# Kernel tuning notes

Hardware: AMD Instinct MI355X
Metric: run time of the kernel (lower is better)

Reference implementation:

```python
import jax, jax.numpy as jnp
import numpy as np
from jax.scipy.special import logsumexp

REG_E = 0.05
N_ITER = 20


def setup_inputs() -> dict:
    key = jax.random.key(0)
    kP, kQ = jax.random.split(key)
    n, m, d = 8192, 8192, 64
    XP = jax.random.normal(kP, (n, d), dtype=jnp.float32)
    XQ = jax.random.normal(kQ, (m, d), dtype=jnp.float32)
    return {"XP": XP, "XQ": XQ}


def sq_cdist(X, Y):
    # squared euclidean distances, (n, m)
    x2 = jnp.sum(X * X, axis=1, keepdims=True)          # (n,1)
    y2 = jnp.sum(Y * Y, axis=1, keepdims=True).T        # (1,m)
    d2 = x2 + y2 - 2.0 * (X @ Y.T)
    return jnp.maximum(d2, 0.0)


def log_sinkhorn(log_a, log_b, C, reg, n_iter):
    # stable log-domain Sinkhorn; returns transport plan exp(M + u[:,None] + v[None,:])
    M = -C / reg                                        # (n,m)
    u0 = jnp.zeros_like(log_a)
    v0 = jnp.zeros_like(log_b)

    def body(carry, _):
        u, v = carry
        u = log_a - logsumexp(M + v[None, :], axis=1)
        v = log_b - logsumexp(M + u[:, None], axis=0)
        return (u, v), None

    (u, v), _ = jax.lax.scan(body, (u0, v0), None, length=n_iter)
    return jnp.exp(M + u[:, None] + v[None, :])


def reference(XP, XQ):
    n, m = XP.shape[0], XQ.shape[0]
    log_uP = jnp.full((n,), -jnp.log(jnp.float32(n)), dtype=XP.dtype)
    log_uQ = jnp.full((m,), -jnp.log(jnp.float32(m)), dtype=XQ.dtype)

    C = sq_cdist(XP, XQ)                                # (n, m)
    Cn = C / jax.lax.stop_gradient(jnp.max(C))
    plan = jax.lax.stop_gradient(
        log_sinkhorn(log_uP, log_uQ, Cn, REG_E, N_ITER)
    )
    return jnp.sum(C * plan)
```

## Files before the change

kernel.cpp:

```cpp
#include <hip/hip_runtime.h>
#include <cmath>

#define NPTS 8192
#define DIM  64
#define LOG2E 1.4426950408889634f
#define LA2   -13.0f

typedef short s16x8  __attribute__((ext_vector_type(8)));
typedef float f32x16 __attribute__((ext_vector_type(16)));

typedef __attribute__((address_space(1))) const unsigned char g8_t;
typedef __attribute__((address_space(3))) unsigned char l8_t;

#if __has_builtin(__builtin_amdgcn_exp2f)
__device__ __forceinline__ float exp2_fast(float x) { return __builtin_amdgcn_exp2f(x); }
#else
__device__ __forceinline__ float exp2_fast(float x) { return exp2f(x); }
#endif
#if __has_builtin(__builtin_amdgcn_logf)
__device__ __forceinline__ float log2_fast(float x) { return __builtin_amdgcn_logf(x); }
#else
__device__ __forceinline__ float log2_fast(float x) { return log2f(x); }
#endif

__device__ __forceinline__ unsigned short f2bf(float x) {
  unsigned u = __float_as_uint(x);
  return (unsigned short)((u + 0x7FFFu + ((u >> 16) & 1u)) >> 16);
}
__device__ __forceinline__ float bf2f(unsigned short b) {
  return __uint_as_float(((unsigned)b) << 16);
}

__global__ __launch_bounds__(256) void prep_kernel(
    const float* __restrict__ XP, const float* __restrict__ XQ,
    unsigned short* __restrict__ Phi, unsigned short* __restrict__ Plo,
    unsigned short* __restrict__ Qhi, unsigned short* __restrict__ Qlo,
    float* __restrict__ x2, float* __restrict__ y2,
    float* __restrict__ scal, float* __restrict__ out) {
  int gid  = blockIdx.x * 256 + threadIdx.x;
  int lane = threadIdx.x & 63;
  int row  = gid >> 6;
  int isP  = row < NPTS;
  int r    = row & (NPTS - 1);
  const float* X = isP ? XP : XQ;
  float x = X[r * DIM + lane];
  unsigned short h = f2bf(x);
  (isP ? Phi : Qhi)[r * DIM + lane] = h;
  (isP ? Plo : Qlo)[r * DIM + lane] = f2bf(x - bf2f(h));
  float s = x * x;
  for (int off = 32; off; off >>= 1) s += __shfl_down(s, off, 64);
  if (lane == 0) (isP ? x2 : y2)[r] = s;
  if (gid == 0) { ((unsigned*)scal)[0] = 0u; out[0] = 0.0f; }
}

template <int MODE, bool FIRST, int MINW>
__global__ __launch_bounds__(256, MINW) void pass_kernel(
    const unsigned short* __restrict__ Ahi, const unsigned short* __restrict__ Alo,
    const unsigned short* __restrict__ Bhi,
    const float* __restrict__ x2row, const float* __restrict__ y2col,
    const float* __restrict__ colPart, const float* __restrict__ rowPart,
    const unsigned* __restrict__ cmaxBits,
    float* __restrict__ outPart, float* __restrict__ outScalar) {
  __shared__ short sB[2][128 * DIM];
  __shared__ float sCol[512];
  __shared__ float sY2[512];
  __shared__ float sX2[128];
  __shared__ float sU2[128];
  __shared__ float sRed[4];

  const int t  = threadIdx.x;
  const int w  = t >> 6;
  const int l  = t & 63;
  const int g  = l >> 5;
  const int ln = l & 31;
  const int i0 = blockIdx.x * 128;
  const int j0 = blockIdx.y * 512;

  float invC = 0.f, C2L = 0.f;
  if constexpr (MODE != 0) {
    float cmax = __uint_as_float(*cmaxBits);
    invC = 1.0f / (0.05f * cmax);
    C2L  = 2.0f * invC * LOG2E;
  }

  const int gOff   = (w * 32 + (l >> 3)) * 128 + (((l & 7) ^ (l >> 3)) * 16);
  const int ldsOff = w * 4096 + l * 16;
  auto stage = [&](int qq, int bi) {
    const unsigned char* src =
        (const unsigned char*)(Bhi + (size_t)(j0 + qq * 128) * DIM) + gOff;
    unsigned char* dst = (unsigned char*)(&sB[bi][0]) + ldsOff;
#pragma unroll
    for (int c = 0; c < 4; ++c)
      __builtin_amdgcn_global_load_lds((g8_t*)(src + c * 1024),
                                       (l8_t*)(dst + c * 1024), 16, 0, 0);
  };

  stage(0, 0);
  stage(1, 1);

  s16x8 a_hi[4], a_lo[4];
  {
    const unsigned short* pa = Ahi + (size_t)(i0 + w * 32 + ln) * DIM + g * 8;
#pragma unroll
    for (int ks = 0; ks < 4; ++ks) a_hi[ks] = *(const s16x8*)(pa + ks * 16);
    if constexpr (MODE == 2) {
      const unsigned short* pb = Alo + (size_t)(i0 + w * 32 + ln) * DIM + g * 8;
#pragma unroll
      for (int ks = 0; ks < 4; ++ks) a_lo[ks] = *(const s16x8*)(pb + ks * 16);
    }
  }

#pragma unroll
  for (int c0 = 0; c0 < 2; ++c0) {
    int c = c0 * 256 + t;
    int j = j0 + c;
    if constexpr (MODE == 0) {
      sY2[c] = y2col[j];
    } else if constexpr (MODE == 1) {
      if constexpr (FIRST) {
        sCol[c] = -invC * y2col[j] * LOG2E;
      } else {
        float s = 0.f;
#pragma unroll
        for (int gy = 0; gy < 16; ++gy) s += colPart[gy * NPTS + j];
        sCol[c] = LA2 - log2_fast(s);
      }
    } else {
      float s = 0.f;
#pragma unroll
      for (int gy = 0; gy < 16; ++gy) s += colPart[gy * NPTS + j];
      sCol[c] = LA2 - log2_fast(s);
      sY2[c] = y2col[j];
    }
  }
  if constexpr (MODE != 1) {
    if (t < 128) {
      sX2[t] = x2row[i0 + t];
      if constexpr (MODE == 2) {
        float s = 0.f;
#pragma unroll
        for (int gy = 0; gy < 16; ++gy) s += rowPart[gy * NPTS + i0 + t];
        sU2[t] = LA2 - log2_fast(s);
      }
    }
  }
  __syncthreads();

  float x2r[16], u2r[16];
  if constexpr (MODE != 1) {
#pragma unroll
    for (int r = 0; r < 16; ++r) {
      int ri = w * 32 + (r & 3) + 8 * (r >> 2) + 4 * g;
      x2r[r] = sX2[ri];
      if constexpr (MODE == 2) u2r[r] = sU2[ri];
    }
  }

  float racc[16];
#pragma unroll
  for (int r = 0; r < 16; ++r) racc[r] = 0.f;
  float accS = 0.f;

  auto do_quarter = [&](const short* __restrict__ buf, int qq) {
#pragma unroll 2
    for (int ct = 0; ct < 4; ++ct) {
      const int nn = ct * 32 + ln;
      const int n  = qq * 128 + ct * 32 + ln;
      s16x8 b[4];
#pragma unroll
      for (int ks = 0; ks < 4; ++ks)
        b[ks] = *(const s16x8*)(buf + nn * DIM + (((ks * 2 + g) ^ (ln & 7)) * 8));
      f32x16 acc;
#pragma unroll
      for (int r = 0; r < 16; ++r) acc[r] = 0.f;
#pragma unroll
      for (int ks = 0; ks < 4; ++ks)
        acc = __builtin_amdgcn_mfma_f32_32x32x16_bf16(a_hi[ks], b[ks], acc, 0, 0, 0);

      if constexpr (MODE == 1) {
        const float bb = sCol[n];
#pragma unroll
        for (int r = 0; r < 16; ++r)
          racc[r] += exp2_fast(fmaf(C2L, acc[r], bb));
      } else if constexpr (MODE == 0) {
        const float y2v = sY2[n];
#pragma unroll
        for (int r = 0; r < 16; ++r)
          accS = fmaxf(accS, fmaf(-2.0f, acc[r], x2r[r] + y2v));
      } else {
        f32x16 acc2;
#pragma unroll
        for (int r = 0; r < 16; ++r) acc2[r] = 0.f;
#pragma unroll
        for (int ks = 0; ks < 4; ++ks)
          acc2 = __builtin_amdgcn_mfma_f32_32x32x16_bf16(a_lo[ks], b[ks], acc2, 0, 0, 0);
        const float y2v = sY2[n];
        const float bb  = sCol[n];
#pragma unroll
        for (int r = 0; r < 16; ++r) {
          float dot = acc[r] + acc2[r];
          float d2  = fmaxf(fmaf(-2.0f, dot, x2r[r] + y2v), 0.0f);
          accS = fmaf(d2, exp2_fast(fmaf(C2L, dot, u2r[r] + bb)), accS);
        }
      }
    }
  };

  do_quarter(sB[0], 0);
  __syncthreads();
  stage(2, 0);
  do_quarter(sB[1], 1);
  __syncthreads();
  stage(3, 1);
  do_quarter(sB[0], 2);
  __syncthreads();
  do_quarter(sB[1], 3);

  if constexpr (MODE == 1) {
#pragma unroll
    for (int r = 0; r < 16; ++r) {
      float v = racc[r];
      v += __shfl_xor(v, 1, 64);
      v += __shfl_xor(v, 2, 64);
      v += __shfl_xor(v, 4, 64);
      v += __shfl_xor(v, 8, 64);
      v += __shfl_xor(v, 16, 64);
      if (ln == 0)
        outPart[blockIdx.y * NPTS + i0 + w * 32 +
                (r & 3) + 8 * (r >> 2) + 4 * g] = v;
    }
  } else {
    float v = accS;
#pragma unroll
    for (int off = 1; off < 64; off <<= 1) {
      float o = __shfl_xor(v, off, 64);
      v = (MODE == 0) ? fmaxf(v, o) : (v + o);
    }
    if (l == 0) sRed[w] = v;
    __syncthreads();
    if (t == 0) {
      float r0 = (MODE == 0) ? fmaxf(fmaxf(sRed[0], sRed[1]), fmaxf(sRed[2], sRed[3]))
                             : (sRed[0] + sRed[1] + sRed[2] + sRed[3]);
      if constexpr (MODE == 0)
        atomicMax((unsigned*)outScalar, __float_as_uint(r0));
      else
        atomicAdd(outScalar, r0);
    }
  }
}

extern "C" void kernel_launch(void* const* d_in, const int* in_sizes, int n_in,
                              void* d_out, int out_size, void* d_ws, size_t ws_size,
                              hipStream_t stream) {
  (void)in_sizes; (void)n_in; (void)out_size; (void)ws_size;
  const float* XP = (const float*)d_in[0];
  const float* XQ = (const float*)d_in[1];
  float* out = (float*)d_out;

  float* ws    = (float*)d_ws;
  float* x2    = ws;
  float* y2    = ws + 8192;
  float* partU = ws + 16384;
  float* partV = partU + 16 * NPTS;
  float* scal  = partV + 16 * NPTS;
  unsigned short* Phi = (unsigned short*)(scal + 16);
  unsigned short* Plo = Phi + (size_t)NPTS * DIM;
  unsigned short* Qhi = Plo + (size_t)NPTS * DIM;
  unsigned short* Qlo = Qhi + (size_t)NPTS * DIM;

  const unsigned* cmaxB = (const unsigned*)scal;
  dim3 grid(NPTS / 128, NPTS / 512);

  prep_kernel<<<NPTS * 2 * DIM / 256, 256, 0, stream>>>(
      XP, XQ, Phi, Plo, Qhi, Qlo, x2, y2, scal, out);

  pass_kernel<0, false, 4><<<grid, 256, 0, stream>>>(
      Phi, nullptr, Qhi, x2, y2, nullptr, nullptr, cmaxB, nullptr, scal);

  pass_kernel<1, true, 4><<<grid, 256, 0, stream>>>(
      Phi, nullptr, Qhi, nullptr, y2, nullptr, nullptr, cmaxB, partU, nullptr);
  pass_kernel<1, false, 4><<<grid, 256, 0, stream>>>(
      Qhi, nullptr, Phi, nullptr, nullptr, partU, nullptr, cmaxB, partV, nullptr);

  for (int it = 1; it < 20; ++it) {
    pass_kernel<1, false, 4><<<grid, 256, 0, stream>>>(
        Phi, nullptr, Qhi, nullptr, nullptr, partV, nullptr, cmaxB, partU, nullptr);
    pass_kernel<1, false, 4><<<grid, 256, 0, stream>>>(
        Qhi, nullptr, Phi, nullptr, nullptr, partU, nullptr, cmaxB, partV, nullptr);
  }

  pass_kernel<2, false, 2><<<grid, 256, 0, stream>>>(
      Phi, Plo, Qhi, x2, y2, partV, partU, cmaxB, nullptr, out);
}
```

Measured before the change: 820.2 us.

## Process two row strips per block to reuse staged column tiles

Each block of the distance-max and Sinkhorn passes now covers 256 rows instead of 128. It keeps two sets of A fragments and row accumulators in registers, so each B tile loaded into LDS and read into registers feeds twice the MFMA work. The grid for those passes is halved and the launch-bounds occupancy hint drops from 4 to 2, trading fewer waves and more registers for less LDS staging and LDS reads per output. The final weighted-sum pass keeps the single-strip layout.

```diff
diff --git a/kernel.cpp b/kernel.cpp
--- a/kernel.cpp
+++ b/kernel.cpp
@@ -53,7 +53,7 @@
   if (gid == 0) { ((unsigned*)scal)[0] = 0u; out[0] = 0.0f; }
 }
 
-template <int MODE, bool FIRST, int MINW>
+template <int MODE, bool FIRST, int MINW, int STRIPS>
 __global__ __launch_bounds__(256, MINW) void pass_kernel(
     const unsigned short* __restrict__ Ahi, const unsigned short* __restrict__ Alo,
     const unsigned short* __restrict__ Bhi,
@@ -64,7 +64,7 @@
   __shared__ short sB[2][128 * DIM];
   __shared__ float sCol[512];
   __shared__ float sY2[512];
-  __shared__ float sX2[128];
+  __shared__ float sX2[256];
   __shared__ float sU2[128];
   __shared__ float sRed[4];
 
@@ -73,7 +73,7 @@
   const int l  = t & 63;
   const int g  = l >> 5;
   const int ln = l & 31;
-  const int i0 = blockIdx.x * 128;
+  const int i0 = blockIdx.x * (128 * STRIPS);
   const int j0 = blockIdx.y * 512;
 
   float invC = 0.f, C2L = 0.f;
@@ -98,15 +98,18 @@
   stage(0, 0);
   stage(1, 1);
 
-  s16x8 a_hi[4], a_lo[4];
-  {
-    const unsigned short* pa = Ahi + (size_t)(i0 + w * 32 + ln) * DIM + g * 8;
-#pragma unroll
-    for (int ks = 0; ks < 4; ++ks) a_hi[ks] = *(const s16x8*)(pa + ks * 16);
+  s16x8 a_hi[STRIPS][4], a_lo[STRIPS][4];
+#pragma unroll
+  for (int s = 0; s < STRIPS; ++s) {
+    const unsigned short* pa =
+        Ahi + (size_t)(i0 + s * 128 + w * 32 + ln) * DIM + g * 8;
+#pragma unroll
+    for (int ks = 0; ks < 4; ++ks) a_hi[s][ks] = *(const s16x8*)(pa + ks * 16);
     if constexpr (MODE == 2) {
-      const unsigned short* pb = Alo + (size_t)(i0 + w * 32 + ln) * DIM + g * 8;
-#pragma unroll
-      for (int ks = 0; ks < 4; ++ks) a_lo[ks] = *(const s16x8*)(pb + ks * 16);
+      const unsigned short* pb =
+          Alo + (size_t)(i0 + s * 128 + w * 32 + ln) * DIM + g * 8;
+#pragma unroll
+      for (int ks = 0; ks < 4; ++ks) a_lo[s][ks] = *(const s16x8*)(pb + ks * 16);
     }
   }
 
@@ -134,7 +137,7 @@
     }
   }
   if constexpr (MODE != 1) {
-    if (t < 128) {
+    if (t < 128 * STRIPS) {
       sX2[t] = x2row[i0 + t];
       if constexpr (MODE == 2) {
         float s = 0.f;
@@ -146,19 +149,23 @@
   }
   __syncthreads();
 
-  float x2r[16], u2r[16];
+  float x2r[STRIPS][16], u2r[STRIPS][16];
   if constexpr (MODE != 1) {
 #pragma unroll
-    for (int r = 0; r < 16; ++r) {
-      int ri = w * 32 + (r & 3) + 8 * (r >> 2) + 4 * g;
-      x2r[r] = sX2[ri];
-      if constexpr (MODE == 2) u2r[r] = sU2[ri];
-    }
-  }
-
-  float racc[16];
-#pragma unroll
-  for (int r = 0; r < 16; ++r) racc[r] = 0.f;
+    for (int s = 0; s < STRIPS; ++s)
+#pragma unroll
+      for (int r = 0; r < 16; ++r) {
+        int ri = s * 128 + w * 32 + (r & 3) + 8 * (r >> 2) + 4 * g;
+        x2r[s][r] = sX2[ri];
+        if constexpr (MODE == 2) u2r[s][r] = sU2[ri];
+      }
+  }
+
+  float racc[STRIPS][16];
+#pragma unroll
+  for (int s = 0; s < STRIPS; ++s)
+#pragma unroll
+    for (int r = 0; r < 16; ++r) racc[s][r] = 0.f;
   float accS = 0.f;
 
   auto do_quarter = [&](const short* __restrict__ buf, int qq) {
@@ -170,37 +177,40 @@
 #pragma unroll
       for (int ks = 0; ks < 4; ++ks)
         b[ks] = *(const s16x8*)(buf + nn * DIM + (((ks * 2 + g) ^ (ln & 7)) * 8));
-      f32x16 acc;
-#pragma unroll
-      for (int r = 0; r < 16; ++r) acc[r] = 0.f;
-#pragma unroll
-      for (int ks = 0; ks < 4; ++ks)
-        acc = __builtin_amdgcn_mfma_f32_32x32x16_bf16(a_hi[ks], b[ks], acc, 0, 0, 0);
-
-      if constexpr (MODE == 1) {
-        const float bb = sCol[n];
-#pragma unroll
-        for (int r = 0; r < 16; ++r)
-          racc[r] += exp2_fast(fmaf(C2L, acc[r], bb));
-      } else if constexpr (MODE == 0) {
-        const float y2v = sY2[n];
-#pragma unroll
-        for (int r = 0; r < 16; ++r)
-          accS = fmaxf(accS, fmaf(-2.0f, acc[r], x2r[r] + y2v));
-      } else {
-        f32x16 acc2;
-#pragma unroll
-        for (int r = 0; r < 16; ++r) acc2[r] = 0.f;
+#pragma unroll
+      for (int s = 0; s < STRIPS; ++s) {
+        f32x16 acc;
+#pragma unroll
+        for (int r = 0; r < 16; ++r) acc[r] = 0.f;
 #pragma unroll
         for (int ks = 0; ks < 4; ++ks)
-          acc2 = __builtin_amdgcn_mfma_f32_32x32x16_bf16(a_lo[ks], b[ks], acc2, 0, 0, 0);
-        const float y2v = sY2[n];
-        const float bb  = sCol[n];
-#pragma unroll
-        for (int r = 0; r < 16; ++r) {
-          float dot = acc[r] + acc2[r];
-          float d2  = fmaxf(fmaf(-2.0f, dot, x2r[r] + y2v), 0.0f);
-          accS = fmaf(d2, exp2_fast(fmaf(C2L, dot, u2r[r] + bb)), accS);
+          acc = __builtin_amdgcn_mfma_f32_32x32x16_bf16(a_hi[s][ks], b[ks], acc, 0, 0, 0);
+
+        if constexpr (MODE == 1) {
+          const float bb = sCol[n];
+#pragma unroll
+          for (int r = 0; r < 16; ++r)
+            racc[s][r] += exp2_fast(fmaf(C2L, acc[r], bb));
+        } else if constexpr (MODE == 0) {
+          const float y2v = sY2[n];
+#pragma unroll
+          for (int r = 0; r < 16; ++r)
+            accS = fmaxf(accS, fmaf(-2.0f, acc[r], x2r[s][r] + y2v));
+        } else {
+          f32x16 acc2;
+#pragma unroll
+          for (int r = 0; r < 16; ++r) acc2[r] = 0.f;
+#pragma unroll
+          for (int ks = 0; ks < 4; ++ks)
+            acc2 = __builtin_amdgcn_mfma_f32_32x32x16_bf16(a_lo[s][ks], b[ks], acc2, 0, 0, 0);
+          const float y2v = sY2[n];
+          const float bb  = sCol[n];
+#pragma unroll
+          for (int r = 0; r < 16; ++r) {
+            float dot = acc[r] + acc2[r];
+            float d2  = fmaxf(fmaf(-2.0f, dot, x2r[s][r] + y2v), 0.0f);
+            accS = fmaf(d2, exp2_fast(fmaf(C2L, dot, u2r[s][r] + bb)), accS);
+          }
         }
       }
     }
@@ -218,17 +228,19 @@
 
   if constexpr (MODE == 1) {
 #pragma unroll
-    for (int r = 0; r < 16; ++r) {
-      float v = racc[r];
-      v += __shfl_xor(v, 1, 64);
-      v += __shfl_xor(v, 2, 64);
-      v += __shfl_xor(v, 4, 64);
-      v += __shfl_xor(v, 8, 64);
-      v += __shfl_xor(v, 16, 64);
-      if (ln == 0)
-        outPart[blockIdx.y * NPTS + i0 + w * 32 +
-                (r & 3) + 8 * (r >> 2) + 4 * g] = v;
-    }
+    for (int s = 0; s < STRIPS; ++s)
+#pragma unroll
+      for (int r = 0; r < 16; ++r) {
+        float v = racc[s][r];
+        v += __shfl_xor(v, 1, 64);
+        v += __shfl_xor(v, 2, 64);
+        v += __shfl_xor(v, 4, 64);
+        v += __shfl_xor(v, 8, 64);
+        v += __shfl_xor(v, 16, 64);
+        if (ln == 0)
+          outPart[blockIdx.y * NPTS + i0 + s * 128 + w * 32 +
+                  (r & 3) + 8 * (r >> 2) + 4 * g] = v;
+      }
   } else {
     float v = accS;
 #pragma unroll
@@ -269,26 +281,27 @@
   unsigned short* Qlo = Qhi + (size_t)NPTS * DIM;
 
   const unsigned* cmaxB = (const unsigned*)scal;
-  dim3 grid(NPTS / 128, NPTS / 512);
+  dim3 grid2(NPTS / 256, NPTS / 512);
+  dim3 grid1(NPTS / 128, NPTS / 512);
 
   prep_kernel<<<NPTS * 2 * DIM / 256, 256, 0, stream>>>(
       XP, XQ, Phi, Plo, Qhi, Qlo, x2, y2, scal, out);
 
-  pass_kernel<0, false, 4><<<grid, 256, 0, stream>>>(
+  pass_kernel<0, false, 2, 2><<<grid2, 256, 0, stream>>>(
       Phi, nullptr, Qhi, x2, y2, nullptr, nullptr, cmaxB, nullptr, scal);
 
-  pass_kernel<1, true, 4><<<grid, 256, 0, stream>>>(
+  pass_kernel<1, true, 2, 2><<<grid2, 256, 0, stream>>>(
       Phi, nullptr, Qhi, nullptr, y2, nullptr, nullptr, cmaxB, partU, nullptr);
-  pass_kernel<1, false, 4><<<grid, 256, 0, stream>>>(
+  pass_kernel<1, false, 2, 2><<<grid2, 256, 0, stream>>>(
       Qhi, nullptr, Phi, nullptr, nullptr, partU, nullptr, cmaxB, partV, nullptr);
 
   for (int it = 1; it < 20; ++it) {
-    pass_kernel<1, false, 4><<<grid, 256, 0, stream>>>(
+    pass_kernel<1, false, 2, 2><<<grid2, 256, 0, stream>>>(
         Phi, nullptr, Qhi, nullptr, nullptr, partV, nullptr, cmaxB, partU, nullptr);
-    pass_kernel<1, false, 4><<<grid, 256, 0, stream>>>(
+    pass_kernel<1, false, 2, 2><<<grid2, 256, 0, stream>>>(
         Qhi, nullptr, Phi, nullptr, nullptr, partU, nullptr, cmaxB, partV, nullptr);
   }
 
-  pass_kernel<2, false, 2><<<grid, 256, 0, stream>>>(
+  pass_kernel<2, false, 2, 1><<<grid1, 256, 0, stream>>>(
       Phi, Plo, Qhi, x2, y2, partV, partU, cmaxB, nullptr, out);
 }
```

Result: slower. 943.9 us (+15.1%).

## Split Sinkhorn sum pass into lean kernel with smaller column tiles

Applied to the files above, without the earlier changes.

Moves the Sinkhorn logsumexp pass (MODE 1) into a dedicated sum_kernel that uses half-width column tiles (256 per block), half the LDS, per-k B fragment loads and launch bounds targeting 8 waves per SIMD. The grid doubles in y, so the partial-sum buffers grow from 16 to 32 slices and every consumer now reduces 32 partials. The goal is higher occupancy and less register and LDS pressure, so exp2 work overlaps better with the MFMAs. In exchange there are more partial writes and reads, A-fragment loads are repeated across twice as many blocks, and there is less reuse per block.

```diff
diff --git a/kernel.cpp b/kernel.cpp
--- a/kernel.cpp
+++ b/kernel.cpp
@@ -53,6 +53,112 @@
   if (gid == 0) { ((unsigned*)scal)[0] = 0u; out[0] = 0.0f; }
 }
 
+template <bool FIRST>
+__global__ __launch_bounds__(256, 8) void sum_kernel(
+    const unsigned short* __restrict__ Ahi,
+    const unsigned short* __restrict__ Bhi,
+    const float* __restrict__ y2col,
+    const float* __restrict__ colPart,
+    const unsigned* __restrict__ cmaxBits,
+    float* __restrict__ outPart) {
+  __shared__ short sB[2][64 * DIM];
+  __shared__ float sCol[256];
+
+  const int t  = threadIdx.x;
+  const int w  = t >> 6;
+  const int l  = t & 63;
+  const int g  = l >> 5;
+  const int ln = l & 31;
+  const int i0 = blockIdx.x * 128;
+  const int j0 = blockIdx.y * 256;
+
+  const float cmax = __uint_as_float(*cmaxBits);
+  const float invC = 1.0f / (0.05f * cmax);
+  const float C2L  = 2.0f * invC * LOG2E;
+
+  const int gOff   = (w * 16 + (l >> 3)) * 128 + (((l & 7) ^ (l >> 3)) * 16);
+  const int ldsOff = w * 2048 + l * 16;
+  auto stage = [&](int qq, int bi) {
+    const unsigned char* src =
+        (const unsigned char*)(Bhi + (size_t)(j0 + qq * 64) * DIM) + gOff;
+    unsigned char* dst = (unsigned char*)(&sB[bi][0]) + ldsOff;
+#pragma unroll
+    for (int c = 0; c < 2; ++c)
+      __builtin_amdgcn_global_load_lds((g8_t*)(src + c * 1024),
+                                       (l8_t*)(dst + c * 1024), 16, 0, 0);
+  };
+
+  stage(0, 0);
+  stage(1, 1);
+
+  s16x8 a_hi[4];
+  {
+    const unsigned short* pa = Ahi + (size_t)(i0 + w * 32 + ln) * DIM + g * 8;
+#pragma unroll
+    for (int ks = 0; ks < 4; ++ks) a_hi[ks] = *(const s16x8*)(pa + ks * 16);
+  }
+
+  {
+    int j = j0 + t;
+    if constexpr (FIRST) {
+      sCol[t] = -invC * y2col[j] * LOG2E;
+    } else {
+      float s = 0.f;
+#pragma unroll
+      for (int gy = 0; gy < 32; ++gy) s += colPart[gy * NPTS + j];
+      sCol[t] = LA2 - log2_fast(s);
+    }
+  }
+  __syncthreads();
+
+  float racc[16];
+#pragma unroll
+  for (int r = 0; r < 16; ++r) racc[r] = 0.f;
+
+  auto do_quarter = [&](const short* __restrict__ buf, int qq) {
+#pragma unroll 1
+    for (int ct = 0; ct < 2; ++ct) {
+      const int nn = ct * 32 + ln;
+      const int n  = qq * 64 + ct * 32 + ln;
+      f32x16 acc;
+#pragma unroll
+      for (int r = 0; r < 16; ++r) acc[r] = 0.f;
+#pragma unroll
+      for (int ks = 0; ks < 4; ++ks) {
+        s16x8 b = *(const s16x8*)(buf + nn * DIM + (((ks * 2 + g) ^ (ln & 7)) * 8));
+        acc = __builtin_amdgcn_mfma_f32_32x32x16_bf16(a_hi[ks], b, acc, 0, 0, 0);
+      }
+      const float bb = sCol[n];
+#pragma unroll
+      for (int r = 0; r < 16; ++r)
+        racc[r] += exp2_fast(fmaf(C2L, acc[r], bb));
+    }
+  };
+
+  do_quarter(sB[0], 0);
+  __syncthreads();
+  stage(2, 0);
+  do_quarter(sB[1], 1);
+  __syncthreads();
+  stage(3, 1);
+  do_quarter(sB[0], 2);
+  __syncthreads();
+  do_quarter(sB[1], 3);
+
+#pragma unroll
+  for (int r = 0; r < 16; ++r) {
+    float v = racc[r];
+    v += __shfl_xor(v, 1, 64);
+    v += __shfl_xor(v, 2, 64);
+    v += __shfl_xor(v, 4, 64);
+    v += __shfl_xor(v, 8, 64);
+    v += __shfl_xor(v, 16, 64);
+    if (ln == 0)
+      outPart[blockIdx.y * NPTS + i0 + w * 32 +
+              (r & 3) + 8 * (r >> 2) + 4 * g] = v;
+  }
+}
+
 template <int MODE, bool FIRST, int MINW>
 __global__ __launch_bounds__(256, MINW) void pass_kernel(
     const unsigned short* __restrict__ Ahi, const unsigned short* __restrict__ Alo,
@@ -116,49 +222,33 @@
     int j = j0 + c;
     if constexpr (MODE == 0) {
       sY2[c] = y2col[j];
-    } else if constexpr (MODE == 1) {
-      if constexpr (FIRST) {
-        sCol[c] = -invC * y2col[j] * LOG2E;
-      } else {
-        float s = 0.f;
-#pragma unroll
-        for (int gy = 0; gy < 16; ++gy) s += colPart[gy * NPTS + j];
-        sCol[c] = LA2 - log2_fast(s);
-      }
     } else {
       float s = 0.f;
 #pragma unroll
-      for (int gy = 0; gy < 16; ++gy) s += colPart[gy * NPTS + j];
+      for (int gy = 0; gy < 32; ++gy) s += colPart[gy * NPTS + j];
       sCol[c] = LA2 - log2_fast(s);
       sY2[c] = y2col[j];
     }
   }
-  if constexpr (MODE != 1) {
-    if (t < 128) {
-      sX2[t] = x2row[i0 + t];
-      if constexpr (MODE == 2) {
-        float s = 0.f;
-#pragma unroll
-        for (int gy = 0; gy < 16; ++gy) s += rowPart[gy * NPTS + i0 + t];
-        sU2[t] = LA2 - log2_fast(s);
-      }
+  if (t < 128) {
+    sX2[t] = x2row[i0 + t];
+    if constexpr (MODE == 2) {
+      float s = 0.f;
+#pragma unroll
+      for (int gy = 0; gy < 32; ++gy) s += rowPart[gy * NPTS + i0 + t];
+      sU2[t] = LA2 - log2_fast(s);
     }
   }
   __syncthreads();
 
   float x2r[16], u2r[16];
-  if constexpr (MODE != 1) {
-#pragma unroll
-    for (int r = 0; r < 16; ++r) {
-      int ri = w * 32 + (r & 3) + 8 * (r >> 2) + 4 * g;
-      x2r[r] = sX2[ri];
-      if constexpr (MODE == 2) u2r[r] = sU2[ri];
-    }
-  }
-
-  float racc[16];
-#pragma unroll
-  for (int r = 0; r < 16; ++r) racc[r] = 0.f;
+#pragma unroll
+  for (int r = 0; r < 16; ++r) {
+    int ri = w * 32 + (r & 3) + 8 * (r >> 2) + 4 * g;
+    x2r[r] = sX2[ri];
+    if constexpr (MODE == 2) u2r[r] = sU2[ri];
+  }
+
   float accS = 0.f;
 
   auto do_quarter = [&](const short* __restrict__ buf, int qq) {
@@ -177,12 +267,7 @@
       for (int ks = 0; ks < 4; ++ks)
         acc = __builtin_amdgcn_mfma_f32_32x32x16_bf16(a_hi[ks], b[ks], acc, 0, 0, 0);
 
-      if constexpr (MODE == 1) {
-        const float bb = sCol[n];
-#pragma unroll
-        for (int r = 0; r < 16; ++r)
-          racc[r] += exp2_fast(fmaf(C2L, acc[r], bb));
-      } else if constexpr (MODE == 0) {
+      if constexpr (MODE == 0) {
         const float y2v = sY2[n];
 #pragma unroll
         for (int r = 0; r < 16; ++r)
@@ -216,36 +301,21 @@
   __syncthreads();
   do_quarter(sB[1], 3);
 
-  if constexpr (MODE == 1) {
-#pragma unroll
-    for (int r = 0; r < 16; ++r) {
-      float v = racc[r];
-      v += __shfl_xor(v, 1, 64);
-      v += __shfl_xor(v, 2, 64);
-      v += __shfl_xor(v, 4, 64);
-      v += __shfl_xor(v, 8, 64);
-      v += __shfl_xor(v, 16, 64);
-      if (ln == 0)
-        outPart[blockIdx.y * NPTS + i0 + w * 32 +
-                (r & 3) + 8 * (r >> 2) + 4 * g] = v;
-    }
-  } else {
-    float v = accS;
-#pragma unroll
-    for (int off = 1; off < 64; off <<= 1) {
-      float o = __shfl_xor(v, off, 64);
-      v = (MODE == 0) ? fmaxf(v, o) : (v + o);
-    }
-    if (l == 0) sRed[w] = v;
-    __syncthreads();
-    if (t == 0) {
-      float r0 = (MODE == 0) ? fmaxf(fmaxf(sRed[0], sRed[1]), fmaxf(sRed[2], sRed[3]))
-                             : (sRed[0] + sRed[1] + sRed[2] + sRed[3]);
-      if constexpr (MODE == 0)
-        atomicMax((unsigned*)outScalar, __float_as_uint(r0));
-      else
-        atomicAdd(outScalar, r0);
-    }
+  float v = accS;
+#pragma unroll
+  for (int off = 1; off < 64; off <<= 1) {
+    float o = __shfl_xor(v, off, 64);
+    v = (MODE == 0) ? fmaxf(v, o) : (v + o);
+  }
+  if (l == 0) sRed[w] = v;
+  __syncthreads();
+  if (t == 0) {
+    float r0 = (MODE == 0) ? fmaxf(fmaxf(sRed[0], sRed[1]), fmaxf(sRed[2], sRed[3]))
+                           : (sRed[0] + sRed[1] + sRed[2] + sRed[3]);
+    if constexpr (MODE == 0)
+      atomicMax((unsigned*)outScalar, __float_as_uint(r0));
+    else
+      atomicAdd(outScalar, r0);
   }
 }
 
@@ -261,34 +331,35 @@
   float* x2    = ws;
   float* y2    = ws + 8192;
   float* partU = ws + 16384;
-  float* partV = partU + 16 * NPTS;
-  float* scal  = partV + 16 * NPTS;
+  float* partV = partU + 32 * NPTS;
+  float* scal  = partV + 32 * NPTS;
   unsigned short* Phi = (unsigned short*)(scal + 16);
   unsigned short* Plo = Phi + (size_t)NPTS * DIM;
   unsigned short* Qhi = Plo + (size_t)NPTS * DIM;
   unsigned short* Qlo = Qhi + (size_t)NPTS * DIM;
 
   const unsigned* cmaxB = (const unsigned*)scal;
-  dim3 grid(NPTS / 128, NPTS / 512);
+  dim3 gridW(NPTS / 128, NPTS / 512);
+  dim3 gridN(NPTS / 128, NPTS / 256);
 
   prep_kernel<<<NPTS * 2 * DIM / 256, 256, 0, stream>>>(
       XP, XQ, Phi, Plo, Qhi, Qlo, x2, y2, scal, out);
 
-  pass_kernel<0, false, 4><<<grid, 256, 0, stream>>>(
+  pass_kernel<0, false, 4><<<gridW, 256, 0, stream>>>(
       Phi, nullptr, Qhi, x2, y2, nullptr, nullptr, cmaxB, nullptr, scal);
 
-  pass_kernel<1, true, 4><<<grid, 256, 0, stream>>>(
-      Phi, nullptr, Qhi, nullptr, y2, nullptr, nullptr, cmaxB, partU, nullptr);
-  pass_kernel<1, false, 4><<<grid, 256, 0, stream>>>(
-      Qhi, nullptr, Phi, nullptr, nullptr, partU, nullptr, cmaxB, partV, nullptr);
+  sum_kernel<true><<<gridN, 256, 0, stream>>>(
+      Phi, Qhi, y2, nullptr, cmaxB, partU);
+  sum_kernel<false><<<gridN, 256, 0, stream>>>(
+      Qhi, Phi, nullptr, partU, cmaxB, partV);
 
   for (int it = 1; it < 20; ++it) {
-    pass_kernel<1, false, 4><<<grid, 256, 0, stream>>>(
-        Phi, nullptr, Qhi, nullptr, nullptr, partV, nullptr, cmaxB, partU, nullptr);
-    pass_kernel<1, false, 4><<<grid, 256, 0, stream>>>(
-        Qhi, nullptr, Phi, nullptr, nullptr, partU, nullptr, cmaxB, partV, nullptr);
-  }
-
-  pass_kernel<2, false, 2><<<grid, 256, 0, stream>>>(
+    sum_kernel<false><<<gridN, 256, 0, stream>>>(
+        Phi, Qhi, nullptr, partV, cmaxB, partU);
+    sum_kernel<false><<<gridN, 256, 0, stream>>>(
+        Qhi, Phi, nullptr, partU, cmaxB, partV);
+  }
+
+  pass_kernel<2, false, 2><<<gridW, 256, 0, stream>>>(
       Phi, Plo, Qhi, x2, y2, partV, partU, cmaxB, nullptr, out);
 }
```

New measurement: 952.1 us. 1.16x slower.
